# Performance work log

Measured on AMD Instinct MI355X. Metric: run time of the kernel, lower is better.

The kernel has to match this reference:

```python
import jax, jax.numpy as jnp
import numpy as np

B, HI, WI, DIM = 16, 64, 64, 256
HEADS, HEAD_DIM, NUM_MEM = 8, 32, 4
HID = HEADS * HEAD_DIM


def setup_inputs() -> dict:
    key = jax.random.key(0)
    ks = jax.random.split(key, 6)
    return {
        "x": jax.random.normal(ks[0], (B, HI, WI, DIM), jnp.float32),
        "gamma_in": jax.random.normal(ks[1], (DIM,), jnp.float32) * 0.02,
        "w_qkv": jax.random.normal(ks[2], (DIM, 3 * HID), jnp.float32) / np.sqrt(DIM),
        "b_qkv": jnp.zeros((3 * HID,), jnp.float32),
        "mem_kv": jax.random.normal(ks[3], (2, HEADS, NUM_MEM, HEAD_DIM), jnp.float32),
        "w_out": jax.random.normal(ks[4], (HID, DIM), jnp.float32) / np.sqrt(HID),
        "b_out": jnp.zeros((DIM,), jnp.float32),
        "gamma_out": jax.random.normal(ks[5], (DIM,), jnp.float32) * 0.02,
    }


def reference(x, gamma_in, w_qkv, b_qkv, mem_kv, w_out, b_out, gamma_out):
    b, h, w, c = x.shape
    n = h * w
    rms_scale = c ** 0.5
    attn_scale = HEAD_DIM ** -0.5

    # RMSNorm (as written in source: pure learned scaling)
    xn = x * (gamma_in + 1.0) * rms_scale

    # 1x1 conv == per-pixel linear projection
    qkv = xn @ w_qkv + b_qkv                       # (b, h, w, 3*HID)
    q, k, v = jnp.split(qkv, 3, axis=-1)

    def to_heads(t):                                # (b,h,w,HID) -> (b, heads, d, n)
        return t.reshape(b, n, HEADS, HEAD_DIM).transpose(0, 2, 3, 1)

    q, k, v = map(to_heads, (q, k, v))

    # memory kv: (heads, m, d) -> (b, heads, d, m), concat along sequence axis
    mk = jnp.broadcast_to(mem_kv[0].transpose(0, 2, 1)[None], (b, HEADS, HEAD_DIM, NUM_MEM))
    mv = jnp.broadcast_to(mem_kv[1].transpose(0, 2, 1)[None], (b, HEADS, HEAD_DIM, NUM_MEM))
    k = jnp.concatenate([mk, k], axis=-1)           # (b, heads, d, n+m)
    v = jnp.concatenate([mv, v], axis=-1)

    # feature-map attention: softmax q over feature dim, k over sequence dim
    q = jax.nn.softmax(q * attn_scale, axis=-2)     # source scales q before softmax
    k = jax.nn.softmax(k, axis=-1)

    context = jnp.einsum('bhdn,bhen->bhde', k, v)   # (b, heads, d, e) small
    out = jnp.einsum('bhde,bhdn->bhen', context, q) # (b, heads, e, n)

    out = out.transpose(0, 3, 1, 2).reshape(b, h, w, HID)
    y = out @ w_out + b_out                         # 1x1 output conv
    return y * (gamma_out + 1.0) * rms_scale        # output RMSNorm
```

## Files before the change

### kernel.cpp

```cpp
#include <hip/hip_runtime.h>
#include <hip/hip_bf16.h>

typedef __bf16 bf16_t;
typedef _Float16 fp16_t;
typedef _Float16 f16x8 __attribute__((ext_vector_type(8)));
typedef __bf16 bf16x8 __attribute__((ext_vector_type(8)));
typedef float f32x4 __attribute__((ext_vector_type(4)));

#define ATTN_SCALE 0.17677669529663687f
#define K_SHIFT 64.0f
#define Q_SHIFT 8.0f

__device__ __forceinline__ void gload16(const void* g, void* l) {
  __builtin_amdgcn_global_load_lds((const __attribute__((address_space(1))) void*)g,
                                   (__attribute__((address_space(3))) void*)l, 16, 0, 0);
}

__global__ __launch_bounds__(256) void prep_pack(
    const float* __restrict__ w_qkv, fp16_t* __restrict__ Bpack) {
  int idx = blockIdx.x * 256 + threadIdx.x;
  int l = idx & 63;
  int rest = idx >> 6;
  int f = rest & 3;
  int kk = (rest >> 2) & 7;
  int nt = rest >> 5;
  int n = nt * 64 + f * 16 + (l & 15);
  int k0 = kk * 32 + (l >> 4) * 8;
  f16x8 v;
#pragma unroll
  for (int e = 0; e < 8; ++e) v[e] = (fp16_t)w_qkv[(k0 + e) * 768 + n];
  ((f16x8*)Bpack)[idx] = v;
}

__global__ __launch_bounds__(256) void gemm_qvk_ctx(
    const float* __restrict__ x, const float* __restrict__ gamma_in,
    const fp16_t* __restrict__ Bpack, const float* __restrict__ bias,
    fp16_t* __restrict__ qe_out, float* __restrict__ part) {
  __shared__ fp16_t A[64 * 256];
  __shared__ bf16_t Pl[128 * 64];
  __shared__ bf16_t Vl[128 * 64];
  int t = threadIdx.x, l = t & 63, w = t >> 6;
  int lr = l >> 4, lc = l & 15;
  int bx = blockIdx.x;
  int m0 = bx * 64;

#pragma unroll
  for (int i = 0; i < 8; ++i) {
    int idx = i * 256 + t;
    int r = idx >> 5, c8 = idx & 31;
    const float* src = x + (size_t)(m0 + r) * 256 + c8 * 8;
    const float* gsc = gamma_in + c8 * 8;
    f16x8 hv;
#pragma unroll
    for (int j = 0; j < 8; ++j) hv[j] = (fp16_t)(src[j] * (gsc[j] + 1.f) * 16.f);
    *(f16x8*)&A[r * 256 + ((c8 ^ (r & 31)) * 8)] = hv;
  }
  __syncthreads();

  auto run_unit = [&](int nt, f32x4 acc[4][4]) {
    const fp16_t* Bp = Bpack + (size_t)nt * 16384;
#pragma unroll
    for (int mf = 0; mf < 4; ++mf)
#pragma unroll
      for (int nf = 0; nf < 4; ++nf) acc[mf][nf] = (f32x4){0.f, 0.f, 0.f, 0.f};
#pragma unroll
    for (int kk = 0; kk < 8; ++kk) {
      f16x8 af[4], bfr[4];
#pragma unroll
      for (int f = 0; f < 4; ++f) {
        int ra = f * 16 + lc;
        af[f] = *(const f16x8*)&A[ra * 256 + (((kk * 4 + lr) ^ (ra & 31)) * 8)];
        bfr[f] = *(const f16x8*)(Bp + (size_t)(kk * 4 + f) * 512 + l * 8);
      }
#pragma unroll
      for (int mf = 0; mf < 4; ++mf)
#pragma unroll
        for (int nf = 0; nf < 4; ++nf)
          acc[mf][nf] = __builtin_amdgcn_mfma_f32_16x16x32_f16(af[mf], bfr[nf], acc[mf][nf], 0, 0, 0);
    }
  };

  {
    f32x4 acc[4][4];
    run_unit(w, acc);
    int n0 = w * 64;
    float bq[4];
#pragma unroll
    for (int nf = 0; nf < 4; ++nf) bq[nf] = bias[n0 + nf * 16 + lc];
#pragma unroll
    for (int mf = 0; mf < 4; ++mf)
#pragma unroll
      for (int r = 0; r < 4; ++r) {
        int row = m0 + mf * 16 + lr * 4 + r;
#pragma unroll
        for (int nf = 0; nf < 4; ++nf) {
          float ql = (acc[mf][nf][r] + bq[nf]) * ATTN_SCALE;
          qe_out[(size_t)row * 256 + n0 + nf * 16 + lc] = (fp16_t)__expf(ql - Q_SHIFT);
        }
      }
  }

  bool isK = (w < 2);
  int wu = w & 1;
  for (int ph = 0; ph < 2; ++ph) {
    f32x4 acc[4][4];
    int nt = (isK ? 4 : 8) + ph * 2 + wu;
    run_unit(nt, acc);
    int n0 = nt * 64;
    float bv[4];
#pragma unroll
    for (int nf = 0; nf < 4; ++nf) bv[nf] = bias[n0 + nf * 16 + lc];
#pragma unroll
    for (int mf = 0; mf < 4; ++mf)
#pragma unroll
      for (int r = 0; r < 4; ++r) {
        int row = mf * 16 + lr * 4 + r;
#pragma unroll
        for (int nf = 0; nf < 4; ++nf) {
          float val = acc[mf][nf][r] + bv[nf];
          int col = wu * 64 + nf * 16 + lc;
          int addr = col * 64 + ((((row >> 3) ^ (col & 7)) << 3) | (row & 7));
          if (isK) Pl[addr] = (bf16_t)__expf(val - K_SHIFT);
          else     Vl[addr] = (bf16_t)val;
        }
      }
    __syncthreads();

    {
      int hb = w * 32;
      f32x4 sacc[2][2];
      f32x4 zacc[2];
#pragma unroll
      for (int mf = 0; mf < 2; ++mf) {
#pragma unroll
        for (int nf = 0; nf < 2; ++nf) sacc[mf][nf] = (f32x4){0.f, 0.f, 0.f, 0.f};
        zacc[mf] = (f32x4){0.f, 0.f, 0.f, 0.f};
      }
      bf16x8 ones;
#pragma unroll
      for (int i = 0; i < 8; ++i) ones[i] = (bf16_t)1.0f;
#pragma unroll
      for (int kk = 0; kk < 2; ++kk) {
        bf16x8 ap[2], bvv[2];
#pragma unroll
        for (int mf = 0; mf < 2; ++mf) {
          int colA = hb + mf * 16 + lc;
          ap[mf] = *(const bf16x8*)&Pl[colA * 64 + (((kk * 4 + lr) ^ (colA & 7)) << 3)];
          bvv[mf] = *(const bf16x8*)&Vl[colA * 64 + (((kk * 4 + lr) ^ (colA & 7)) << 3)];
        }
#pragma unroll
        for (int mf = 0; mf < 2; ++mf) {
#pragma unroll
          for (int nf = 0; nf < 2; ++nf)
            sacc[mf][nf] = __builtin_amdgcn_mfma_f32_16x16x32_bf16(ap[mf], bvv[nf], sacc[mf][nf], 0, 0, 0);
          zacc[mf] = __builtin_amdgcn_mfma_f32_16x16x32_bf16(ap[mf], ones, zacc[mf], 0, 0, 0);
        }
      }
      float* pp = part + (size_t)bx * 8448 + (ph * 4 + w) * 1056;
#pragma unroll
      for (int mf = 0; mf < 2; ++mf)
#pragma unroll
        for (int r = 0; r < 4; ++r) {
          int dd = mf * 16 + lr * 4 + r;
#pragma unroll
          for (int nf = 0; nf < 2; ++nf) pp[dd * 32 + nf * 16 + lc] = sacc[mf][nf][r];
          if (lc == 0) pp[1024 + dd] = zacc[mf][r];
        }
    }
    __syncthreads();
  }
}

__global__ __launch_bounds__(256) void build_wt(
    const float* __restrict__ part, const float* __restrict__ w_out,
    const float* __restrict__ mem_kv, fp16_t* __restrict__ Bpacky) {
  int bh = blockIdx.x;
  int b = bh >> 3, h = bh & 7;
  int t = threadIdx.x;
  __shared__ float S[32][32];
  __shared__ float Zr[32];
  __shared__ float W[32][256];
  for (int idx = t; idx < 1024; idx += 256) {
    float s = 0.f;
    for (int c = 0; c < 64; ++c) s += part[((size_t)(b * 64 + c)) * 8448 + h * 1056 + idx];
    S[idx >> 5][idx & 31] = s;
  }
  if (t < 32) {
    float zz = 0.f;
    for (int c = 0; c < 64; ++c) zz += part[((size_t)(b * 64 + c)) * 8448 + h * 1056 + 1024 + t];
    Zr[t] = zz;
  }
  for (int i = t; i < 32 * 256; i += 256) W[i >> 8][i & 255] = w_out[(h * 32 + (i >> 8)) * 256 + (i & 255)];
  __syncthreads();
  if (t < 32) {
    int dd = t;
    for (int m = 0; m < 4; ++m) {
      float p = __expf(mem_kv[h * 128 + m * 32 + dd] - K_SHIFT);
      Zr[dd] += p;
      for (int e = 0; e < 32; ++e) S[dd][e] += p * mem_kv[1024 + h * 128 + m * 32 + e];
    }
  }
  __syncthreads();
  int c = t;
  int nt = c >> 6, f = (c >> 4) & 3, lc = c & 15;
  for (int dd = 0; dd < 32; ++dd) {
    float acc = 0;
#pragma unroll 8
    for (int e = 0; e < 32; ++e) acc += S[dd][e] * W[e][c];
    int kcol = h * 32 + dd;
    int kk = kcol >> 5, lr = (kcol & 31) >> 3, e8 = kcol & 7;
    size_t addr = ((((size_t)(b * 4 + nt) * 8 + kk) * 4 + f) * 64 + (lr * 16 + lc)) * 8 + e8;
    Bpacky[addr] = (fp16_t)(acc / Zr[dd]);
  }
}

__global__ __launch_bounds__(256) void gemm_y(
    const fp16_t* __restrict__ qe, const fp16_t* __restrict__ Bpacky,
    const float* __restrict__ b_out, const float* __restrict__ gamma_out,
    float* __restrict__ y_out) {
  __shared__ fp16_t A[64 * 256];
  __shared__ float zbuf[64][8];
  int t = threadIdx.x, l = t & 63, w = t >> 6;
  int lr = l >> 4, lc = l & 15;
  int m0 = blockIdx.x * 64;
#pragma unroll
  for (int i = 0; i < 8; ++i) {
    int idx = i * 256 + t;
    int r = idx >> 5, cs = idx & 31;
    gload16(qe + (size_t)(m0 + r) * 256 + ((cs ^ (r & 31)) * 8), &A[idx * 8]);
  }
  __syncthreads();

#pragma unroll
  for (int pi = 0; pi < 2; ++pi) {
    int p = pi * 256 + t;
    int r = p >> 3, hh = p & 7;
    float zs = 0.f;
#pragma unroll
    for (int c = 0; c < 4; ++c) {
      int cs = (hh * 4 + c) ^ (r & 31);
      f16x8 vv = *(const f16x8*)&A[r * 256 + cs * 8];
#pragma unroll
      for (int j = 0; j < 8; ++j) zs += (float)vv[j];
    }
    zbuf[r][hh] = 1.f / zs;
  }
  __syncthreads();

#pragma unroll
  for (int i = 0; i < 8; ++i) {
    int idx = i * 256 + t;
    int r = idx >> 5, cs = idx & 31;
    int hh = (cs ^ (r & 31)) >> 2;
    float sc = zbuf[r][hh];
    f16x8 vv = *(const f16x8*)&A[idx * 8];
#pragma unroll
    for (int j = 0; j < 8; ++j) vv[j] = (fp16_t)((float)vv[j] * sc);
    *(f16x8*)&A[idx * 8] = vv;
  }
  __syncthreads();

  int n0 = w * 64;
  const fp16_t* Bp = Bpacky + (size_t)(m0 >> 12) * 65536 + (size_t)w * 16384;
  f32x4 acc[4][4];
#pragma unroll
  for (int mf = 0; mf < 4; ++mf)
#pragma unroll
    for (int nf = 0; nf < 4; ++nf) acc[mf][nf] = (f32x4){0.f, 0.f, 0.f, 0.f};
#pragma unroll
  for (int kk = 0; kk < 8; ++kk) {
    f16x8 af[4], bfr[4];
#pragma unroll
    for (int f = 0; f < 4; ++f) {
      int ra = f * 16 + lc;
      af[f] = *(const f16x8*)&A[ra * 256 + (((kk * 4 + lr) ^ (ra & 31)) * 8)];
      bfr[f] = *(const f16x8*)(Bp + (size_t)(kk * 4 + f) * 512 + l * 8);
    }
#pragma unroll
    for (int mf = 0; mf < 4; ++mf)
#pragma unroll
      for (int nf = 0; nf < 4; ++nf)
        acc[mf][nf] = __builtin_amdgcn_mfma_f32_16x16x32_f16(af[mf], bfr[nf], acc[mf][nf], 0, 0, 0);
  }
  float bv[4], gv[4];
#pragma unroll
  for (int nf = 0; nf < 4; ++nf) {
    int c = n0 + nf * 16 + lc;
    bv[nf] = b_out[c];
    gv[nf] = (gamma_out[c] + 1.f) * 16.f;
  }
#pragma unroll
  for (int mf = 0; mf < 4; ++mf)
#pragma unroll
    for (int r = 0; r < 4; ++r) {
      int row = m0 + mf * 16 + lr * 4 + r;
#pragma unroll
      for (int nf = 0; nf < 4; ++nf)
        y_out[(size_t)row * 256 + n0 + nf * 16 + lc] = (acc[mf][nf][r] + bv[nf]) * gv[nf];
    }
}

extern "C" void kernel_launch(void* const* d_in, const int* in_sizes, int n_in,
                              void* d_out, int out_size, void* d_ws, size_t ws_size,
                              hipStream_t stream) {
  const float* x        = (const float*)d_in[0];
  const float* gamma_in = (const float*)d_in[1];
  const float* w_qkv    = (const float*)d_in[2];
  const float* b_qkv    = (const float*)d_in[3];
  const float* mem_kv   = (const float*)d_in[4];
  const float* w_out    = (const float*)d_in[5];
  const float* b_out    = (const float*)d_in[6];
  const float* gamma_out= (const float*)d_in[7];
  float* y = (float*)d_out;

  char* ws = (char*)d_ws;
  fp16_t* qe     = (fp16_t*)(ws);
  fp16_t* Bpack  = (fp16_t*)(ws + 33554432);
  fp16_t* Bpacky = (fp16_t*)(ws + 33947648);
  float*  part   = (float*)(ws + 36044800);

  prep_pack<<<96, 256, 0, stream>>>(w_qkv, Bpack);
  gemm_qvk_ctx<<<1024, 256, 0, stream>>>(x, gamma_in, Bpack, b_qkv, qe, part);
  build_wt<<<128, 256, 0, stream>>>(part, w_out, mem_kv, Bpacky);
  gemm_y<<<1024, 256, 0, stream>>>(qe, Bpacky, b_out, gamma_out, y);
}
```

Before: 125.1 us.

## Split K/V projection into four phases with half-size LDS tiles

The K/V projection stage now runs in four phases of one 64-column tile each, with each wave computing 32 rows instead of 64. This halves the P and V shared-memory buffers and the accumulator register count, which is meant to raise occupancy. The context MFMA work is split across waves by column half, and results are written to LDS as packed bf16x4 stores. In exchange, B-fragment loads from global memory are repeated across waves, and each block now does four barrier-separated phases instead of two.

```diff
diff --git a/kernel.cpp b/kernel.cpp
--- a/kernel.cpp
+++ b/kernel.cpp
@@ -5,6 +5,7 @@
 typedef _Float16 fp16_t;
 typedef _Float16 f16x8 __attribute__((ext_vector_type(8)));
 typedef __bf16 bf16x8 __attribute__((ext_vector_type(8)));
+typedef __bf16 bf16x4 __attribute__((ext_vector_type(4)));
 typedef float f32x4 __attribute__((ext_vector_type(4)));
 
 #define ATTN_SCALE 0.17677669529663687f
@@ -37,8 +38,8 @@
     const fp16_t* __restrict__ Bpack, const float* __restrict__ bias,
     fp16_t* __restrict__ qe_out, float* __restrict__ part) {
   __shared__ fp16_t A[64 * 256];
-  __shared__ bf16_t Pl[128 * 64];
-  __shared__ bf16_t Vl[128 * 64];
+  __shared__ bf16_t Pl[64 * 64];
+  __shared__ bf16_t Vl[64 * 64];
   int t = threadIdx.x, l = t & 63, w = t >> 6;
   int lr = l >> 4, lc = l & 15;
   int bx = blockIdx.x;
@@ -57,8 +58,9 @@
   }
   __syncthreads();
 
-  auto run_unit = [&](int nt, f32x4 acc[4][4]) {
-    const fp16_t* Bp = Bpack + (size_t)nt * 16384;
+  {
+    const fp16_t* Bp = Bpack + (size_t)w * 16384;
+    f32x4 acc[4][4];
 #pragma unroll
     for (int mf = 0; mf < 4; ++mf)
 #pragma unroll
@@ -78,11 +80,6 @@
         for (int nf = 0; nf < 4; ++nf)
           acc[mf][nf] = __builtin_amdgcn_mfma_f32_16x16x32_f16(af[mf], bfr[nf], acc[mf][nf], 0, 0, 0);
     }
-  };
-
-  {
-    f32x4 acc[4][4];
-    run_unit(w, acc);
     int n0 = w * 64;
     float bq[4];
 #pragma unroll
@@ -101,39 +98,64 @@
   }
 
   bool isK = (w < 2);
-  int wu = w & 1;
-  for (int ph = 0; ph < 2; ++ph) {
-    f32x4 acc[4][4];
-    int nt = (isK ? 4 : 8) + ph * 2 + wu;
-    run_unit(nt, acc);
+  int rh = w & 1;
+  int hq = w & 1;
+  int chalf = w >> 1;
+  for (int ph = 0; ph < 4; ++ph) {
+    int nt = (isK ? 4 : 8) + ph;
+    const fp16_t* Bp = Bpack + (size_t)nt * 16384;
+    f32x4 acc[2][4];
+#pragma unroll
+    for (int mf = 0; mf < 2; ++mf)
+#pragma unroll
+      for (int nf = 0; nf < 4; ++nf) acc[mf][nf] = (f32x4){0.f, 0.f, 0.f, 0.f};
+#pragma unroll
+    for (int kk = 0; kk < 8; ++kk) {
+      f16x8 af[2], bfr[4];
+#pragma unroll
+      for (int f = 0; f < 2; ++f) {
+        int ra = rh * 32 + f * 16 + lc;
+        af[f] = *(const f16x8*)&A[ra * 256 + (((kk * 4 + lr) ^ (ra & 31)) * 8)];
+      }
+#pragma unroll
+      for (int f = 0; f < 4; ++f)
+        bfr[f] = *(const f16x8*)(Bp + (size_t)(kk * 4 + f) * 512 + l * 8);
+#pragma unroll
+      for (int mf = 0; mf < 2; ++mf)
+#pragma unroll
+        for (int nf = 0; nf < 4; ++nf)
+          acc[mf][nf] = __builtin_amdgcn_mfma_f32_16x16x32_f16(af[mf], bfr[nf], acc[mf][nf], 0, 0, 0);
+    }
     int n0 = nt * 64;
     float bv[4];
 #pragma unroll
     for (int nf = 0; nf < 4; ++nf) bv[nf] = bias[n0 + nf * 16 + lc];
 #pragma unroll
-    for (int mf = 0; mf < 4; ++mf)
-#pragma unroll
-      for (int r = 0; r < 4; ++r) {
-        int row = mf * 16 + lr * 4 + r;
-#pragma unroll
-        for (int nf = 0; nf < 4; ++nf) {
+    for (int mf = 0; mf < 2; ++mf) {
+#pragma unroll
+      for (int nf = 0; nf < 4; ++nf) {
+        int col = nf * 16 + lc;
+        int row0 = rh * 32 + mf * 16 + lr * 4;
+        bf16x4 pk;
+#pragma unroll
+        for (int r = 0; r < 4; ++r) {
           float val = acc[mf][nf][r] + bv[nf];
-          int col = wu * 64 + nf * 16 + lc;
-          int addr = col * 64 + ((((row >> 3) ^ (col & 7)) << 3) | (row & 7));
-          if (isK) Pl[addr] = (bf16_t)__expf(val - K_SHIFT);
-          else     Vl[addr] = (bf16_t)val;
-        }
-      }
+          pk[r] = isK ? (bf16_t)__expf(val - K_SHIFT) : (bf16_t)val;
+        }
+        int addr = col * 64 + ((((row0 >> 3) ^ (col & 7)) << 3) | (row0 & 7));
+        if (isK) *(bf16x4*)&Pl[addr] = pk;
+        else     *(bf16x4*)&Vl[addr] = pk;
+      }
+    }
     __syncthreads();
 
     {
-      int hb = w * 32;
-      f32x4 sacc[2][2];
+      int hb = hq * 32;
+      f32x4 sacc[2];
       f32x4 zacc[2];
 #pragma unroll
       for (int mf = 0; mf < 2; ++mf) {
-#pragma unroll
-        for (int nf = 0; nf < 2; ++nf) sacc[mf][nf] = (f32x4){0.f, 0.f, 0.f, 0.f};
+        sacc[mf] = (f32x4){0.f, 0.f, 0.f, 0.f};
         zacc[mf] = (f32x4){0.f, 0.f, 0.f, 0.f};
       }
       bf16x8 ones;
@@ -141,30 +163,29 @@
       for (int i = 0; i < 8; ++i) ones[i] = (bf16_t)1.0f;
 #pragma unroll
       for (int kk = 0; kk < 2; ++kk) {
-        bf16x8 ap[2], bvv[2];
+        bf16x8 ap[2], bvv;
 #pragma unroll
         for (int mf = 0; mf < 2; ++mf) {
           int colA = hb + mf * 16 + lc;
           ap[mf] = *(const bf16x8*)&Pl[colA * 64 + (((kk * 4 + lr) ^ (colA & 7)) << 3)];
-          bvv[mf] = *(const bf16x8*)&Vl[colA * 64 + (((kk * 4 + lr) ^ (colA & 7)) << 3)];
-        }
+        }
+        int colB = hb + chalf * 16 + lc;
+        bvv = *(const bf16x8*)&Vl[colB * 64 + (((kk * 4 + lr) ^ (colB & 7)) << 3)];
 #pragma unroll
         for (int mf = 0; mf < 2; ++mf) {
-#pragma unroll
-          for (int nf = 0; nf < 2; ++nf)
-            sacc[mf][nf] = __builtin_amdgcn_mfma_f32_16x16x32_bf16(ap[mf], bvv[nf], sacc[mf][nf], 0, 0, 0);
-          zacc[mf] = __builtin_amdgcn_mfma_f32_16x16x32_bf16(ap[mf], ones, zacc[mf], 0, 0, 0);
-        }
-      }
-      float* pp = part + (size_t)bx * 8448 + (ph * 4 + w) * 1056;
+          sacc[mf] = __builtin_amdgcn_mfma_f32_16x16x32_bf16(ap[mf], bvv, sacc[mf], 0, 0, 0);
+          if (chalf == 0)
+            zacc[mf] = __builtin_amdgcn_mfma_f32_16x16x32_bf16(ap[mf], ones, zacc[mf], 0, 0, 0);
+        }
+      }
+      float* pp = part + (size_t)bx * 8448 + (ph * 2 + hq) * 1056;
 #pragma unroll
       for (int mf = 0; mf < 2; ++mf)
 #pragma unroll
         for (int r = 0; r < 4; ++r) {
           int dd = mf * 16 + lr * 4 + r;
-#pragma unroll
-          for (int nf = 0; nf < 2; ++nf) pp[dd * 32 + nf * 16 + lc] = sacc[mf][nf][r];
-          if (lc == 0) pp[1024 + dd] = zacc[mf][r];
+          pp[dd * 32 + chalf * 16 + lc] = sacc[mf][r];
+          if (chalf == 0 && lc == 0) pp[1024 + dd] = zacc[mf][r];
         }
     }
     __syncthreads();
```

New measurement: 128.1 us. 1.02x slower.
